# Performance work log

Measured on AMD Instinct MI355X. Metric: run time of the kernel, lower is better.

Reference implementation:

```python
import jax, jax.numpy as jnp
import numpy as np

B, N, M, K = 2, 65536, 8192, 32
N_CY = N_CONE = N_DISK = N_ELLIP = 16
TOTAL_GIBS = N_CY + N_CONE + N_DISK + N_ELLIP
NUM_OBSERVERS = 16
KERNEL_REACH = 1.0
EPS = 1e-8


def setup_inputs() -> dict:
    key = jax.random.key(0)
    ks = jax.random.split(key, 10)
    points = jax.random.normal(ks[0], (B, N, 3), dtype=jnp.float32)
    q_coords = jax.random.normal(ks[1], (B, M, 3), dtype=jnp.float32)
    support_idxs = jax.random.randint(ks[2], (B, M, K), 0, N)
    mc_points = jax.random.normal(ks[3], (1024, 3), dtype=jnp.float32)
    # per-GIB geometric params, positive, within kernel reach (random_init analogue)
    u = lambda k, shp: 0.1 + (KERNEL_REACH - 0.1) * jax.random.uniform(k, shp, dtype=jnp.float32)
    cy_params = u(ks[4], (N_CY, 2))      # [radius, sigma]
    cone_params = u(ks[5], (N_CONE, 2))  # [slope, sigma]
    disk_params = u(ks[6], (N_DISK, 2))  # [radius, height]
    ellip_params = u(ks[7], (N_ELLIP, 3))  # [rx, ry, rz]
    # cvx coefficients: softmax over GIB axis (maintain_convexity at init)
    lambdas = jax.nn.softmax(jax.random.normal(ks[8], (TOTAL_GIBS, NUM_OBSERVERS), dtype=jnp.float32), axis=0)
    return {"points": points, "q_coords": q_coords, "support_idxs": support_idxs,
            "mc_points": mc_points, "cy_params": cy_params, "cone_params": cone_params,
            "disk_params": disk_params, "ellip_params": ellip_params, "lambdas": lambdas}


def _gib_outputs(points, q_coords, support_idxs, cy_p, cone_p, disk_p, ellip_p):
    # shared neighborhood gather: (B, M, K, 3)
    supp = points[jnp.arange(points.shape[0])[:, None, None], support_idxs]
    rel = supp - q_coords[:, :, None, :]
    rx, ry, rz = rel[..., 0], rel[..., 1], rel[..., 2]
    r2 = rx * rx + ry * ry                     # (B, M, K) squared radial dist
    r2e, rze = r2[..., None], rz[..., None]    # (B, M, K, 1)
    # cylinder: gaussian shell around radius in the xy-plane
    cy = jnp.exp(-(r2e - cy_p[:, 0] ** 2) ** 2 / (2.0 * cy_p[:, 1] ** 2 + EPS))
    # cone: radial distance tracks slope * height
    cone = jnp.exp(-(jnp.sqrt(r2e + EPS) - cone_p[:, 0] * rze) ** 2 / (2.0 * cone_p[:, 1] ** 2 + EPS))
    # disk: flattened gaussian (wide radially, thin in z)
    disk = jnp.exp(-r2e / (disk_p[:, 0] ** 2 + EPS) - rze ** 2 / (disk_p[:, 1] ** 2 + EPS))
    # ellipsoid: anisotropic gaussian
    el = jnp.exp(-(rx[..., None] ** 2 / (ellip_p[:, 0] ** 2 + EPS)
                   + ry[..., None] ** 2 / (ellip_p[:, 1] ** 2 + EPS)
                   + rz[..., None] ** 2 / (ellip_p[:, 2] ** 2 + EPS)))
    # reduce over neighborhood K, then stack GIBs: (B, M, total_gibs)
    return jnp.concatenate([cy.mean(axis=2), cone.mean(axis=2),
                            disk.mean(axis=2), el.mean(axis=2)], axis=-1)


def reference(points, q_coords, support_idxs, mc_points, cy_params, cone_params,
              disk_params, ellip_params, lambdas):
    q_out = _gib_outputs(points, q_coords, support_idxs,
                         cy_params, cone_params, disk_params, ellip_params)
    # observers: convex combination of GIB responses -> (B, M, num_observers)
    return q_out @ lambdas
```

## Files before the change

### kernel.cpp

```cpp
#include <hip/hip_runtime.h>


#define EPSF 1e-8f
#define LOG2E 1.4426950408889634f

constexpr int QPB         = 16;
constexpr int GEO_QSTRIDE = 264;
constexpr int LAM_STRIDE  = 20;

__global__ __launch_bounds__(256, 4) void gib_kernel(
    const float* __restrict__ points,
    const float* __restrict__ qc,
    const int*   __restrict__ sidx,
    const float* __restrict__ cyp,
    const float* __restrict__ conep,
    const float* __restrict__ diskp,
    const float* __restrict__ ellp,
    const float* __restrict__ lam,
    float*       __restrict__ out)
{
    __shared__ float  geo[QPB * GEO_QSTRIDE];
    __shared__ float  lamS[64 * LAM_STRIDE];
    __shared__ float4 pkA[16];
    __shared__ float4 pkB[16];
    __shared__ float  pkC[16];

    const int tid = threadIdx.x;

    if (tid < 16) {
        float c0 = cyp[2 * tid], c1 = cyp[2 * tid + 1];
        float k0 = conep[2 * tid], k1 = conep[2 * tid + 1];
        float d0 = diskp[2 * tid], d1 = diskp[2 * tid + 1];
        float e0 = ellp[3 * tid], e1 = ellp[3 * tid + 1], e2 = ellp[3 * tid + 2];
        pkA[tid] = make_float4(c0 * c0, -LOG2E / (2.f * c1 * c1 + EPSF),
                               k0,      -LOG2E / (2.f * k1 * k1 + EPSF));
        pkB[tid] = make_float4(-LOG2E / (d0 * d0 + EPSF), -LOG2E / (d1 * d1 + EPSF),
                               -LOG2E / (e0 * e0 + EPSF), -LOG2E / (e1 * e1 + EPSF));
        pkC[tid] = -LOG2E / (e2 * e2 + EPSF);
    }

    {
        int g = tid >> 2, c = (tid & 3) * 4;
#pragma unroll
        for (int j = 0; j < 4; j++)
            lamS[g * LAM_STRIDE + c + j] = lam[g * 16 + c + j] * (1.0f / 32.0f);
    }

#pragma unroll
    for (int it = 0; it < 2; it++) {
        int i  = tid + it * 256;
        int ql = i >> 5, k = i & 31;
        int qg = blockIdx.x * QPB + ql;
        int b  = qg >> 13;
        int idx = sidx[qg * 32 + k];
        const float* pp = points + ((size_t)(b << 16) + idx) * 3;
        const float* qq = qc + qg * 3;
        float rx = pp[0] - qq[0];
        float ry = pp[1] - qq[1];
        float rz = pp[2] - qq[2];
        float rx2 = rx * rx, ry2 = ry * ry, rz2 = rz * rz;
        float r2 = rx2 + ry2;
        float s  = sqrtf(r2 + EPSF);
        float* gp = &geo[ql * GEO_QSTRIDE + k * 8];
        *(float4*)gp       = make_float4(r2, s, rz, rx2);
        *(float4*)(gp + 4) = make_float4(ry2, rz2, 0.f, 0.f);
    }
    __syncthreads();

    const int l  = tid & 63;
    const int ql = (tid >> 6) * 4 + (l >> 4);
    const int lg = l & 15;

    const float4 pA = pkA[lg];
    const float4 pB = pkB[lg];
    const float  eC = pkC[lg];

    float a0 = 0.f, a1 = 0.f, a2 = 0.f, a3 = 0.f;
    const float* gq = &geo[ql * GEO_QSTRIDE];
#pragma unroll 8
    for (int k = 0; k < 32; k++) {
        float4 ga = *(const float4*)(gq + k * 8);
        float2 gb = *(const float2*)(gq + k * 8 + 4);
        float r2 = ga.x, s = ga.y, rz = ga.z, rx2 = ga.w;
        float ry2 = gb.x, rz2 = gb.y;
        float t = r2 - pA.x;
        a0 += exp2f(t * t * pA.y);
        float u = fmaf(-pA.z, rz, s);
        a1 += exp2f(u * u * pA.w);
        a2 += exp2f(fmaf(r2, pB.x, rz2 * pB.y));
        a3 += exp2f(fmaf(rx2, pB.z, fmaf(ry2, pB.w, rz2 * eC)));
    }

    float sv[16];
#pragma unroll
    for (int i = 0; i < 16; i++) sv[i] = 0.f;
    const float accs[4] = {a0, a1, a2, a3};
#pragma unroll
    for (int t = 0; t < 4; t++) {
        const float* lrow = &lamS[(t * 16 + lg) * LAM_STRIDE];
        float4 L0 = *(const float4*)(lrow);
        float4 L1 = *(const float4*)(lrow + 4);
        float4 L2 = *(const float4*)(lrow + 8);
        float4 L3 = *(const float4*)(lrow + 12);
        float a = accs[t];
        sv[0]  = fmaf(a, L0.x, sv[0]);
        sv[8]  = fmaf(a, L0.y, sv[8]);
        sv[4]  = fmaf(a, L0.z, sv[4]);
        sv[12] = fmaf(a, L0.w, sv[12]);
        sv[2]  = fmaf(a, L1.x, sv[2]);
        sv[10] = fmaf(a, L1.y, sv[10]);
        sv[6]  = fmaf(a, L1.z, sv[6]);
        sv[14] = fmaf(a, L1.w, sv[14]);
        sv[1]  = fmaf(a, L2.x, sv[1]);
        sv[9]  = fmaf(a, L2.y, sv[9]);
        sv[5]  = fmaf(a, L2.z, sv[5]);
        sv[13] = fmaf(a, L2.w, sv[13]);
        sv[3]  = fmaf(a, L3.x, sv[3]);
        sv[11] = fmaf(a, L3.y, sv[11]);
        sv[7]  = fmaf(a, L3.z, sv[7]);
        sv[15] = fmaf(a, L3.w, sv[15]);
    }

    {
        bool up = (lg & 1);
#pragma unroll
        for (int i = 0; i < 8; i++) {
            float keep = up ? sv[i + 8] : sv[i];
            float send = up ? sv[i] : sv[i + 8];
            sv[i] = keep + __shfl_xor(send, 1, 64);
        }
    }
    {
        bool up = (lg & 2);
#pragma unroll
        for (int i = 0; i < 4; i++) {
            float keep = up ? sv[i + 4] : sv[i];
            float send = up ? sv[i] : sv[i + 4];
            sv[i] = keep + __shfl_xor(send, 2, 64);
        }
    }
    {
        bool up = (lg & 4);
#pragma unroll
        for (int i = 0; i < 2; i++) {
            float keep = up ? sv[i + 2] : sv[i];
            float send = up ? sv[i] : sv[i + 2];
            sv[i] = keep + __shfl_xor(send, 4, 64);
        }
    }
    {
        bool up = (lg & 8);
        float keep = up ? sv[1] : sv[0];
        float send = up ? sv[0] : sv[1];
        sv[0] = keep + __shfl_xor(send, 8, 64);
    }

    const int qg = blockIdx.x * QPB + ql;
    out[qg * 16 + lg] = sv[0];
}

extern "C" void kernel_launch(void* const* d_in, const int* in_sizes, int n_in,
                              void* d_out, int out_size, void* d_ws, size_t ws_size,
                              hipStream_t stream) {
    const float* points = (const float*)d_in[0];
    const float* qc     = (const float*)d_in[1];
    const int*   sidx   = (const int*)d_in[2];
    const float* cyp    = (const float*)d_in[4];
    const float* conep  = (const float*)d_in[5];
    const float* diskp  = (const float*)d_in[6];
    const float* ellp   = (const float*)d_in[7];
    const float* lam    = (const float*)d_in[8];
    float*       out    = (float*)d_out;

    const int totalQ = 2 * 8192;
    dim3 grid(totalQ / QPB), block(256);
    hipLaunchKernelGGL(gib_kernel, grid, block, 0, stream,
                       points, qc, sidx, cyp, conep, diskp, ellp, lam, out);
}
```

Measured before the change: 87.02 us.

## Drop shared geometry staging; each lane gathers neighbors and evaluates two GIBs

Removes the shared-memory staging of per-neighbor geometry and the per-block parameter packing. Each lane now handles one pair of GIBs (cylinder+disk or cone+ellipsoid) for one query, gathering all 32 neighbors itself through vectorised index loads and computing rx/ry/rz directly. The loop uses fast amdgcn sqrt/exp2 builtins, and the observer reduction gains an extra xor-16 shuffle. Queries per block drop from 16 to 8 and launch bounds raise the occupancy target. In exchange, each point is gathered redundantly by 32 lanes instead of once, and the cylinder and cone formulas are merged through masking coefficients, which adds FMAs.

```diff
diff --git a/kernel.cpp b/kernel.cpp
--- a/kernel.cpp
+++ b/kernel.cpp
@@ -4,11 +4,9 @@
 #define EPSF 1e-8f
 #define LOG2E 1.4426950408889634f
 
-constexpr int QPB         = 16;
-constexpr int GEO_QSTRIDE = 264;
-constexpr int LAM_STRIDE  = 20;
+constexpr int LAM_STRIDE = 18;
 
-__global__ __launch_bounds__(256, 4) void gib_kernel(
+__global__ __launch_bounds__(256, 8) void gib_kernel(
     const float* __restrict__ points,
     const float* __restrict__ qc,
     const int*   __restrict__ sidx,
@@ -19,110 +17,96 @@
     const float* __restrict__ lam,
     float*       __restrict__ out)
 {
-    __shared__ float  geo[QPB * GEO_QSTRIDE];
-    __shared__ float  lamS[64 * LAM_STRIDE];
-    __shared__ float4 pkA[16];
-    __shared__ float4 pkB[16];
-    __shared__ float  pkC[16];
+    __shared__ float lamS[64 * LAM_STRIDE];
 
     const int tid = threadIdx.x;
 
-    if (tid < 16) {
-        float c0 = cyp[2 * tid], c1 = cyp[2 * tid + 1];
-        float k0 = conep[2 * tid], k1 = conep[2 * tid + 1];
-        float d0 = diskp[2 * tid], d1 = diskp[2 * tid + 1];
-        float e0 = ellp[3 * tid], e1 = ellp[3 * tid + 1], e2 = ellp[3 * tid + 2];
-        pkA[tid] = make_float4(c0 * c0, -LOG2E / (2.f * c1 * c1 + EPSF),
-                               k0,      -LOG2E / (2.f * k1 * k1 + EPSF));
-        pkB[tid] = make_float4(-LOG2E / (d0 * d0 + EPSF), -LOG2E / (d1 * d1 + EPSF),
-                               -LOG2E / (e0 * e0 + EPSF), -LOG2E / (e1 * e1 + EPSF));
-        pkC[tid] = -LOG2E / (e2 * e2 + EPSF);
-    }
-
     {
-        int g = tid >> 2, c = (tid & 3) * 4;
+        int g = tid >> 2, o = (tid & 3) * 4;
 #pragma unroll
         for (int j = 0; j < 4; j++)
-            lamS[g * LAM_STRIDE + c + j] = lam[g * 16 + c + j] * (1.0f / 32.0f);
-    }
-
-#pragma unroll
-    for (int it = 0; it < 2; it++) {
-        int i  = tid + it * 256;
-        int ql = i >> 5, k = i & 31;
-        int qg = blockIdx.x * QPB + ql;
-        int b  = qg >> 13;
-        int idx = sidx[qg * 32 + k];
-        const float* pp = points + ((size_t)(b << 16) + idx) * 3;
-        const float* qq = qc + qg * 3;
-        float rx = pp[0] - qq[0];
-        float ry = pp[1] - qq[1];
-        float rz = pp[2] - qq[2];
-        float rx2 = rx * rx, ry2 = ry * ry, rz2 = rz * rz;
-        float r2 = rx2 + ry2;
-        float s  = sqrtf(r2 + EPSF);
-        float* gp = &geo[ql * GEO_QSTRIDE + k * 8];
-        *(float4*)gp       = make_float4(r2, s, rz, rx2);
-        *(float4*)(gp + 4) = make_float4(ry2, rz2, 0.f, 0.f);
+            lamS[g * LAM_STRIDE + o + j] = lam[g * 16 + o + j] * (1.0f / 32.0f);
     }
     __syncthreads();
 
     const int l  = tid & 63;
-    const int ql = (tid >> 6) * 4 + (l >> 4);
-    const int lg = l & 15;
+    const int c  = l & 31;
+    const int qh = l >> 5;
+    const int q  = blockIdx.x * 8 + (tid >> 6) * 2 + qh;
+    const int b  = q >> 13;
 
-    const float4 pA = pkA[lg];
-    const float4 pB = pkB[lg];
-    const float  eC = pkC[lg];
+    float al1, al2, al3, al4, nb0, A1, B1, C1;
+    if (c < 16) {
+        float c0 = cyp[2 * c], c1 = cyp[2 * c + 1];
+        al1 = 1.f; al2 = 0.f; al3 = 0.f; al4 = -c0 * c0;
+        nb0 = -LOG2E / (2.f * c1 * c1 + EPSF);
+        float d0 = diskp[2 * c], d1 = diskp[2 * c + 1];
+        float ai = -LOG2E / (d0 * d0 + EPSF);
+        A1 = ai; B1 = ai; C1 = -LOG2E / (d1 * d1 + EPSF);
+    } else {
+        int cc = c - 16;
+        float k0 = conep[2 * cc], k1 = conep[2 * cc + 1];
+        al1 = 0.f; al2 = 1.f; al3 = -k0; al4 = 0.f;
+        nb0 = -LOG2E / (2.f * k1 * k1 + EPSF);
+        float e0 = ellp[3 * cc], e1 = ellp[3 * cc + 1], e2 = ellp[3 * cc + 2];
+        A1 = -LOG2E / (e0 * e0 + EPSF);
+        B1 = -LOG2E / (e1 * e1 + EPSF);
+        C1 = -LOG2E / (e2 * e2 + EPSF);
+    }
 
-    float a0 = 0.f, a1 = 0.f, a2 = 0.f, a3 = 0.f;
-    const float* gq = &geo[ql * GEO_QSTRIDE];
-#pragma unroll 8
-    for (int k = 0; k < 32; k++) {
-        float4 ga = *(const float4*)(gq + k * 8);
-        float2 gb = *(const float2*)(gq + k * 8 + 4);
-        float r2 = ga.x, s = ga.y, rz = ga.z, rx2 = ga.w;
-        float ry2 = gb.x, rz2 = gb.y;
-        float t = r2 - pA.x;
-        a0 += exp2f(t * t * pA.y);
-        float u = fmaf(-pA.z, rz, s);
-        a1 += exp2f(u * u * pA.w);
-        a2 += exp2f(fmaf(r2, pB.x, rz2 * pB.y));
-        a3 += exp2f(fmaf(rx2, pB.z, fmaf(ry2, pB.w, rz2 * eC)));
+    const float* qq = qc + q * 3;
+    const float qx = qq[0], qy = qq[1], qz = qq[2];
+    const float* ptbase = points + (size_t)(b << 16) * 3;
+    const int4*  idxp   = (const int4*)(sidx + q * 32);
+
+    float a0 = 0.f, a1 = 0.f;
+#pragma unroll
+    for (int jc = 0; jc < 8; jc++) {
+        const int4 i4 = idxp[jc];
+        const int ii[4] = {i4.x, i4.y, i4.z, i4.w};
+#pragma unroll
+        for (int j = 0; j < 4; j++) {
+            const float* pp = ptbase + ii[j] * 3;
+            float rx = pp[0] - qx;
+            float ry = pp[1] - qy;
+            float rz = pp[2] - qz;
+            float rx2 = rx * rx, ry2 = ry * ry, rz2 = rz * rz;
+            float r2 = rx2 + ry2;
+            float s  = __builtin_amdgcn_sqrtf(r2 + EPSF);
+            float u  = fmaf(al1, r2, fmaf(al2, s, fmaf(al3, rz, al4)));
+            a0 += __builtin_amdgcn_exp2f(u * u * nb0);
+            float v  = fmaf(rx2, A1, fmaf(ry2, B1, rz2 * C1));
+            a1 += __builtin_amdgcn_exp2f(v);
+        }
     }
 
     float sv[16];
-#pragma unroll
-    for (int i = 0; i < 16; i++) sv[i] = 0.f;
-    const float accs[4] = {a0, a1, a2, a3};
-#pragma unroll
-    for (int t = 0; t < 4; t++) {
-        const float* lrow = &lamS[(t * 16 + lg) * LAM_STRIDE];
-        float4 L0 = *(const float4*)(lrow);
-        float4 L1 = *(const float4*)(lrow + 4);
-        float4 L2 = *(const float4*)(lrow + 8);
-        float4 L3 = *(const float4*)(lrow + 12);
-        float a = accs[t];
-        sv[0]  = fmaf(a, L0.x, sv[0]);
-        sv[8]  = fmaf(a, L0.y, sv[8]);
-        sv[4]  = fmaf(a, L0.z, sv[4]);
-        sv[12] = fmaf(a, L0.w, sv[12]);
-        sv[2]  = fmaf(a, L1.x, sv[2]);
-        sv[10] = fmaf(a, L1.y, sv[10]);
-        sv[6]  = fmaf(a, L1.z, sv[6]);
-        sv[14] = fmaf(a, L1.w, sv[14]);
-        sv[1]  = fmaf(a, L2.x, sv[1]);
-        sv[9]  = fmaf(a, L2.y, sv[9]);
-        sv[5]  = fmaf(a, L2.z, sv[5]);
-        sv[13] = fmaf(a, L2.w, sv[13]);
-        sv[3]  = fmaf(a, L3.x, sv[3]);
-        sv[11] = fmaf(a, L3.y, sv[11]);
-        sv[7]  = fmaf(a, L3.z, sv[7]);
-        sv[15] = fmaf(a, L3.w, sv[15]);
+    {
+        const float* ra = &lamS[c * LAM_STRIDE];
+        const float* rb = &lamS[(32 + c) * LAM_STRIDE];
+#define GIB_MV(o, slot) { float2 La = *(const float2*)&ra[o]; float2 Lb = *(const float2*)&rb[o]; \
+        sv[slot##0] = fmaf(a0, La.x, a1 * Lb.x); sv[slot##1] = fmaf(a0, La.y, a1 * Lb.y); }
+        { float2 La = *(const float2*)&ra[0];  float2 Lb = *(const float2*)&rb[0];
+          sv[0]  = fmaf(a0, La.x, a1 * Lb.x); sv[8]  = fmaf(a0, La.y, a1 * Lb.y); }
+        { float2 La = *(const float2*)&ra[2];  float2 Lb = *(const float2*)&rb[2];
+          sv[4]  = fmaf(a0, La.x, a1 * Lb.x); sv[12] = fmaf(a0, La.y, a1 * Lb.y); }
+        { float2 La = *(const float2*)&ra[4];  float2 Lb = *(const float2*)&rb[4];
+          sv[2]  = fmaf(a0, La.x, a1 * Lb.x); sv[10] = fmaf(a0, La.y, a1 * Lb.y); }
+        { float2 La = *(const float2*)&ra[6];  float2 Lb = *(const float2*)&rb[6];
+          sv[6]  = fmaf(a0, La.x, a1 * Lb.x); sv[14] = fmaf(a0, La.y, a1 * Lb.y); }
+        { float2 La = *(const float2*)&ra[8];  float2 Lb = *(const float2*)&rb[8];
+          sv[1]  = fmaf(a0, La.x, a1 * Lb.x); sv[9]  = fmaf(a0, La.y, a1 * Lb.y); }
+        { float2 La = *(const float2*)&ra[10]; float2 Lb = *(const float2*)&rb[10];
+          sv[5]  = fmaf(a0, La.x, a1 * Lb.x); sv[13] = fmaf(a0, La.y, a1 * Lb.y); }
+        { float2 La = *(const float2*)&ra[12]; float2 Lb = *(const float2*)&rb[12];
+          sv[3]  = fmaf(a0, La.x, a1 * Lb.x); sv[11] = fmaf(a0, La.y, a1 * Lb.y); }
+        { float2 La = *(const float2*)&ra[14]; float2 Lb = *(const float2*)&rb[14];
+          sv[7]  = fmaf(a0, La.x, a1 * Lb.x); sv[15] = fmaf(a0, La.y, a1 * Lb.y); }
+#undef GIB_MV
     }
 
     {
-        bool up = (lg & 1);
+        bool up = (c & 1);
 #pragma unroll
         for (int i = 0; i < 8; i++) {
             float keep = up ? sv[i + 8] : sv[i];
@@ -131,7 +115,7 @@
         }
     }
     {
-        bool up = (lg & 2);
+        bool up = (c & 2);
 #pragma unroll
         for (int i = 0; i < 4; i++) {
             float keep = up ? sv[i + 4] : sv[i];
@@ -140,7 +124,7 @@
         }
     }
     {
-        bool up = (lg & 4);
+        bool up = (c & 4);
 #pragma unroll
         for (int i = 0; i < 2; i++) {
             float keep = up ? sv[i + 2] : sv[i];
@@ -149,14 +133,15 @@
         }
     }
     {
-        bool up = (lg & 8);
+        bool up = (c & 8);
         float keep = up ? sv[1] : sv[0];
         float send = up ? sv[0] : sv[1];
         sv[0] = keep + __shfl_xor(send, 8, 64);
     }
+    sv[0] += __shfl_xor(sv[0], 16, 64);
 
-    const int qg = blockIdx.x * QPB + ql;
-    out[qg * 16 + lg] = sv[0];
+    if (c < 16)
+        out[q * 16 + c] = sv[0];
 }
 
 extern "C" void kernel_launch(void* const* d_in, const int* in_sizes, int n_in,
@@ -173,7 +158,7 @@
     float*       out    = (float*)d_out;
 
     const int totalQ = 2 * 8192;
-    dim3 grid(totalQ / QPB), block(256);
+    dim3 grid(totalQ / 8), block(256);
     hipLaunchKernelGGL(gib_kernel, grid, block, 0, stream,
                        points, qc, sidx, cyp, conep, diskp, ellp, lam, out);
 }
```

After: 84.21 us. -3.2%, faster.
